# Optimization experiments

Hardware: AMD Instinct MI355X
Metric: run time of the kernel (lower is better)

## Reference

```python
import jax, jax.numpy as jnp
import numpy as np

SCALE = 1.0 / np.sqrt(2.0).astype(np.float32)  # 1/sqrt(head_dim=2)


def setup_inputs() -> dict:
    key = jax.random.key(0)
    k1, k2 = jax.random.split(key)
    shape = (1, 2048, 8, 2)  # (batch, seq_len, heads, spinor_dim=2)
    return {
        "spinors_real": jax.random.normal(k1, shape, dtype=jnp.float32),
        "spinors_imag": jax.random.normal(k2, shape, dtype=jnp.float32),
    }


def reference(spinors_real, spinors_imag):
    # assemble complex spinors (batch, seq, heads, 2)
    spinors = jax.lax.complex(spinors_real, spinors_imag)
    # L2 norm over the spinor dim (real-valued magnitude norm, as torch.norm on cfloat)
    nrm = jnp.sqrt(jnp.sum(spinors_real * spinors_real + spinors_imag * spinors_imag,
                           axis=-1, keepdims=True))
    normed = spinors / nrm
    # Hermitian inner product logits: (b, i, j, h)
    logits = jnp.einsum('bihd,bjhd->bijh', jnp.conj(normed), normed)
    # softmax over key axis j of the real part, scaled
    attn = jax.nn.softmax(logits.real * SCALE, axis=2)
    # combine original (unnormalized) spinors
    out = jnp.einsum('bijh,bjhd->bihd', attn.astype(spinors.dtype), spinors)
    return out
```

## Files before the change

### kernel.cpp

```cpp
#include <hip/hip_runtime.h>


#define S 2048
#define H 8
#define QR 8

__device__ inline float fast_exp2(float x) {
#if __has_builtin(__builtin_amdgcn_exp2f)
    return __builtin_amdgcn_exp2f(x);
#else
    return exp2f(x);
#endif
}
__device__ inline float2 f2mul(float2 a, float2 b) {
    return make_float2(a.x * b.x, a.y * b.y);
}
__device__ inline float2 f2fma(float2 a, float2 b, float2 c) {
    return make_float2(fmaf(a.x, b.x, c.x), fmaf(a.y, b.y, c.y));
}

__global__ __launch_bounds__(256) void su2_prep(const float* __restrict__ re,
                                                const float* __restrict__ im,
                                                float4* __restrict__ vtab,
                                                float* __restrict__ ntab) {
    int t = blockIdx.x * 256 + threadIdx.x;
    int h = t >> 11;
    int j = t & 2047;
    const float2* re2 = (const float2*)re;
    const float2* im2 = (const float2*)im;
    float2 r = re2[j * H + h];
    float2 m = im2[j * H + h];
    float ss = r.x * r.x + m.x * m.x + r.y * r.y + m.y * m.y;
    vtab[t] = make_float4(r.x, m.x, r.y, m.y);
    ntab[t] = rsqrtf(ss);
}

__global__ __launch_bounds__(256) void su2_attn(const float4* __restrict__ vtab,
                                                const float* __restrict__ ntab,
                                                float2* __restrict__ outr,
                                                float2* __restrict__ outi) {
    const int h    = blockIdx.y;
    const int lane = threadIdx.x & 63;
    const int wave = threadIdx.x >> 6;
    const int i_base = (blockIdx.x * 4 + wave) * QR;

    const float4* __restrict__ vt = vtab + (h << 11);
    const float*  __restrict__ nt = ntab + (h << 11);

    const float c = 0.70710678118654752440f * 1.44269504088896340736f;

    float2 qc0[QR], qc1[QR];
#pragma unroll
    for (int r = 0; r < QR; ++r) {
        float4 v = vt[i_base + r];
        float  s = nt[i_base + r] * c;
        qc0[r] = make_float2(v.x * s, v.y * s);
        qc1[r] = make_float2(v.z * s, v.w * s);
    }

    float  l[QR];
    float2 a0[QR], a1[QR];
#pragma unroll
    for (int r = 0; r < QR; ++r) {
        l[r]  = 0.f;
        a0[r] = make_float2(0.f, 0.f);
        a1[r] = make_float2(0.f, 0.f);
    }

#pragma unroll 4
    for (int jj = 0; jj < S / 64; ++jj) {
        int j = jj * 64 + lane;
        float4 v   = vt[j];
        float  inv = nt[j];
        float2 v0 = make_float2(v.x, v.y);
        float2 v1 = make_float2(v.z, v.w);
#pragma unroll
        for (int r = 0; r < QR; ++r) {
            float2 d2 = f2fma(qc1[r], v1, f2mul(qc0[r], v0));
            float  p  = fast_exp2((d2.x + d2.y) * inv);
            l[r] += p;
            float2 pp = make_float2(p, p);
            a0[r] = f2fma(pp, v0, a0[r]);
            a1[r] = f2fma(pp, v1, a1[r]);
        }
    }

#pragma unroll
    for (int r = 0; r < QR; ++r) {
#pragma unroll
        for (int m = 32; m >= 1; m >>= 1) {
            l[r]    += __shfl_xor(l[r], m, 64);
            a0[r].x += __shfl_xor(a0[r].x, m, 64);
            a0[r].y += __shfl_xor(a0[r].y, m, 64);
            a1[r].x += __shfl_xor(a1[r].x, m, 64);
            a1[r].y += __shfl_xor(a1[r].y, m, 64);
        }
    }

    if (lane == 0) {
#pragma unroll
        for (int r = 0; r < QR; ++r) {
            float invl = 1.0f / l[r];
            int i = i_base + r;
            outr[i * H + h] = make_float2(a0[r].x * invl, a1[r].x * invl);
            outi[i * H + h] = make_float2(a0[r].y * invl, a1[r].y * invl);
        }
    }
}

extern "C" void kernel_launch(void* const* d_in, const int* in_sizes, int n_in,
                              void* d_out, int out_size, void* d_ws, size_t ws_size,
                              hipStream_t stream) {
    const float* re = (const float*)d_in[0];
    const float* im = (const float*)d_in[1];
    float4* vtab = (float4*)d_ws;
    float*  ntab = (float*)(vtab + S * H);
    float2* outr = (float2*)d_out;
    float2* outi = outr + S * H;

    su2_prep<<<dim3(64), dim3(256), 0, stream>>>(re, im, vtab, ntab);
    su2_attn<<<dim3(S / 32, H), dim3(256), 0, stream>>>(vtab, ntab, outr, outi);
}
```

Baseline: 77.71 us.

## Fuse spinor prep into attention kernel using shared-memory key tables

Removes the separate prep kernel and its global workspace tables. Each block now loads the per-head spinors from the raw inputs itself, computes the inverse norms, and stages both in LDS (about 40KB) before the main loop reads keys from shared memory. This removes one kernel launch and the global round trip. In exchange every block redoes the prep for its head, the strided gathers are uncoalesced, and the larger LDS footprint may lower occupancy.

```diff
diff --git a/kernel.cpp b/kernel.cpp
--- a/kernel.cpp
+++ b/kernel.cpp
@@ -19,36 +19,31 @@
     return make_float2(fmaf(a.x, b.x, c.x), fmaf(a.y, b.y, c.y));
 }
 
-__global__ __launch_bounds__(256) void su2_prep(const float* __restrict__ re,
-                                                const float* __restrict__ im,
-                                                float4* __restrict__ vtab,
-                                                float* __restrict__ ntab) {
-    int t = blockIdx.x * 256 + threadIdx.x;
-    int h = t >> 11;
-    int j = t & 2047;
-    const float2* re2 = (const float2*)re;
-    const float2* im2 = (const float2*)im;
-    float2 r = re2[j * H + h];
-    float2 m = im2[j * H + h];
-    float ss = r.x * r.x + m.x * m.x + r.y * r.y + m.y * m.y;
-    vtab[t] = make_float4(r.x, m.x, r.y, m.y);
-    ntab[t] = rsqrtf(ss);
-}
+__global__ __launch_bounds__(256) void su2_attn_fused(
+        const float* __restrict__ re, const float* __restrict__ im,
+        float2* __restrict__ outr, float2* __restrict__ outi) {
+    __shared__ float4 vt[S];
+    __shared__ float  nt[S];
 
-__global__ __launch_bounds__(256) void su2_attn(const float4* __restrict__ vtab,
-                                                const float* __restrict__ ntab,
-                                                float2* __restrict__ outr,
-                                                float2* __restrict__ outi) {
     const int h    = blockIdx.y;
     const int lane = threadIdx.x & 63;
     const int wave = threadIdx.x >> 6;
     const int i_base = (blockIdx.x * 4 + wave) * QR;
 
-    const float4* __restrict__ vt = vtab + (h << 11);
-    const float*  __restrict__ nt = ntab + (h << 11);
+    const float2* __restrict__ re2 = (const float2*)re;
+    const float2* __restrict__ im2 = (const float2*)im;
+#pragma unroll
+    for (int k = 0; k < S / 256; ++k) {
+        int j = k * 256 + threadIdx.x;
+        float2 r = re2[j * H + h];
+        float2 m = im2[j * H + h];
+        float ss = r.x * r.x + m.x * m.x + r.y * r.y + m.y * m.y;
+        vt[j] = make_float4(r.x, m.x, r.y, m.y);
+        nt[j] = rsqrtf(ss);
+    }
+    __syncthreads();
 
     const float c = 0.70710678118654752440f * 1.44269504088896340736f;
-
     float2 qc0[QR], qc1[QR];
 #pragma unroll
     for (int r = 0; r < QR; ++r) {
@@ -113,11 +108,9 @@
                               hipStream_t stream) {
     const float* re = (const float*)d_in[0];
     const float* im = (const float*)d_in[1];
-    float4* vtab = (float4*)d_ws;
-    float*  ntab = (float*)(vtab + S * H);
     float2* outr = (float2*)d_out;
     float2* outi = outr + S * H;
+    (void)d_ws; (void)ws_size;
 
-    su2_prep<<<dim3(64), dim3(256), 0, stream>>>(re, im, vtab, ntab);
-    su2_attn<<<dim3(S / 32, H), dim3(256), 0, stream>>>(vtab, ntab, outr, outi);
+    su2_attn_fused<<<dim3(S / 32, H), dim3(256), 0, stream>>>(re, im, outr, outi);
 }
```

Measured after the change: 72.10 us. 7.2% less time.
